# Kernel tuning notes

Hardware: AMD Instinct MI355X
Metric: run time of the kernel (lower is better)

The kernel has to match this reference:

```python
import jax, jax.numpy as jnp
import numpy as np

N_NODES = 50000
N_EDGES = 1_600_000


def gcn_conv(x, W, b, src, dst, ew, n_nodes):
    """PyG GCNConv: out = D^{-1/2}(A+I)D^{-1/2} (x W) + b, deg from edge_weight,
    self-loop weight = 1. Self-loop term handled analytically (norm = dinv[i]^2)."""
    xW = x @ W                                            # [N, F_out]
    deg = jax.ops.segment_sum(ew, dst, num_segments=n_nodes) + 1.0  # +1 self-loop
    dinv = jnp.where(deg > 0, jax.lax.rsqrt(deg), 0.0)    # [N]
    norm = dinv[src] * ew * dinv[dst]                     # [E]
    agg = jax.ops.segment_sum(norm[:, None] * xW[src], dst, num_segments=n_nodes)
    return agg + (dinv * dinv)[:, None] * xW + b


def setup_inputs() -> dict:
    key = jax.random.key(0)
    ks = jax.random.split(key, 9)
    s = lambda fi, fo: 1.0 / np.sqrt(fi)
    return {
        "x": jax.random.normal(ks[0], (N_NODES, 128), dtype=jnp.float32),
        "edge_index": jax.random.randint(ks[1], (2, N_EDGES), 0, N_NODES, dtype=jnp.int64)
        if jax.config.jax_enable_x64 else jax.random.randint(ks[1], (2, N_EDGES), 0, N_NODES, dtype=jnp.int32),
        "edge_weight": jax.random.uniform(ks[2], (N_EDGES,), dtype=jnp.float32),
        "W1": jax.random.normal(ks[3], (128, 64), dtype=jnp.float32) * s(128, 64),
        "b1": jnp.zeros((64,), dtype=jnp.float32),
        "W2": jax.random.normal(ks[4], (64, 64), dtype=jnp.float32) * s(64, 64),
        "b2": jnp.zeros((64,), dtype=jnp.float32),
        "W3": jax.random.normal(ks[5], (64, 40), dtype=jnp.float32) * s(64, 40),
        "b3": jnp.zeros((40,), dtype=jnp.float32),
    }


def reference(x, edge_index, edge_weight, W1, b1, W2, b2, W3, b3):
    src, dst = edge_index[0], edge_index[1]
    n = x.shape[0]
    h = jax.nn.relu(gcn_conv(x, W1, b1, src, dst, edge_weight, n))
    h = jax.nn.relu(gcn_conv(h, W2, b2, src, dst, edge_weight, n))
    return gcn_conv(h, W3, b3, src, dst, edge_weight, n)
```

## Files before the change

### kernel.cpp

```cpp
#include <hip/hip_runtime.h>


#define TILE 4096
#define BCAP_MAX 9216

typedef int s16i __attribute__((ext_vector_type(16)));

static __device__ __forceinline__ float4 f4zero() { return make_float4(0.f, 0.f, 0.f, 0.f); }

static __device__ __forceinline__ unsigned short f2bf_rne(float x) {
    unsigned u = __float_as_uint(x);
    u += 0x7FFFu + ((u >> 16) & 1u);
    return (unsigned short)(u >> 16);
}
static __device__ __forceinline__ float bf2f(unsigned short b) {
    return __uint_as_float((unsigned)b << 16);
}

__global__ __launch_bounds__(1024) void bin_count_kernel(
        const int* __restrict__ dst, int* __restrict__ cnt, int E, int ntiles) {
    __shared__ int h[256];
    const int tid = threadIdx.x;
    const int t = blockIdx.x;
    if (tid < 256) h[tid] = 0;
    __syncthreads();
    const int e0 = t * TILE;
    #pragma unroll
    for (int j = 0; j < 4; ++j) {
        int e = e0 + j * 1024 + tid;
        if (e < E) atomicAdd(&h[dst[e] >> 8], 1);
    }
    __syncthreads();
    if (tid < 256) cnt[tid * ntiles + t] = h[tid];
}

__global__ __launch_bounds__(512) void bin_scan_kernel(
        int* __restrict__ cnt, int* __restrict__ bintotal, int ntiles) {
    __shared__ int buf[512];
    const int b = blockIdx.x;
    const int tid = threadIdx.x;
    int v = (tid < ntiles) ? cnt[b * ntiles + tid] : 0;
    buf[tid] = v;
    __syncthreads();
    for (int off = 1; off < 512; off <<= 1) {
        int x = buf[tid];
        int a = (tid >= off) ? buf[tid - off] : 0;
        __syncthreads();
        buf[tid] = x + a;
        __syncthreads();
    }
    if (tid < ntiles) cnt[b * ntiles + tid] = buf[tid] - v;
    if (tid == 0) bintotal[b] = buf[511];
}

__global__ __launch_bounds__(1024) void bin_scatter_kernel(
        const int* __restrict__ src, const int* __restrict__ dst,
        const float* __restrict__ ew, const int* __restrict__ cntbase,
        int2* __restrict__ binned, int E, int bcap, int ntiles) {
    __shared__ int cnt[256];
    __shared__ int scan[256];
    __shared__ int gbase[256];
    __shared__ int2 sorted[TILE];
    __shared__ unsigned char binof[TILE];
    const int tid = threadIdx.x;
    const int t = blockIdx.x;
    const int e0 = t * TILE;

    if (tid < 256) cnt[tid] = 0;
    __syncthreads();

    int mypk[4]; float myew[4]; int mybin[4]; int myrank[4]; bool myok[4];
    #pragma unroll
    for (int j = 0; j < 4; ++j) {
        int e = e0 + j * 1024 + tid;
        myok[j] = (e < E);
        if (myok[j]) {
            int d = dst[e];
            int s = src[e];
            myew[j]   = ew[e];
            mybin[j]  = d >> 8;
            mypk[j]   = (s << 8) | (d & 255);
            myrank[j] = atomicAdd(&cnt[mybin[j]], 1);
        }
    }
    __syncthreads();
    if (tid < 256) scan[tid] = cnt[tid];
    __syncthreads();
    for (int off = 1; off < 256; off <<= 1) {
        int v = 0;
        if (tid < 256) { v = scan[tid]; if (tid >= off) v += scan[tid - off]; }
        __syncthreads();
        if (tid < 256) scan[tid] = v;
        __syncthreads();
    }
    if (tid < 256) gbase[tid] = cntbase[tid * ntiles + t];
    __syncthreads();
    #pragma unroll
    for (int j = 0; j < 4; ++j) {
        if (myok[j]) {
            int b = mybin[j];
            int slot = (scan[b] - cnt[b]) + myrank[j];
            sorted[slot] = make_int2(mypk[j], __float_as_int(myew[j]));
            binof[slot]  = (unsigned char)b;
        }
    }
    __syncthreads();
    const int total = scan[255];
    for (int i = tid; i < total; i += 1024) {
        int b = binof[i];
        int pos = gbase[b] + (i - (scan[b] - cnt[b]));
        if (pos < bcap)
            binned[(size_t)b * bcap + pos] = sorted[i];
    }
}

__global__ __launch_bounds__(1024) void bin_group_kernel(
        int2* __restrict__ binned, const int* __restrict__ bintotal,
        int* __restrict__ row_start, int* __restrict__ row_cnt,
        float* __restrict__ dinv, int N, int bcap) {
    __shared__ int   cntl[256];
    __shared__ float degl[256];
    __shared__ int   scan[256];
    __shared__ int   run[256];
    __shared__ int2  sorted[BCAP_MAX];
    const int b = blockIdx.x;
    const int tid = threadIdx.x;
    int n = bintotal[b];
    if (n > bcap) n = bcap;
    if (tid < 256) { cntl[tid] = 0; degl[tid] = 0.f; }
    __syncthreads();

    int2* seg = binned + (size_t)b * bcap;
    for (int i = tid; i < n; i += 1024) {
        int2 v = seg[i];
        int dl = v.x & 255;
        atomicAdd(&cntl[dl], 1);
        atomicAdd(&degl[dl], __int_as_float(v.y));
    }
    __syncthreads();
    if (tid < 256) scan[tid] = cntl[tid];
    __syncthreads();
    for (int off = 1; off < 256; off <<= 1) {
        int v = 0;
        if (tid < 256) { v = scan[tid]; if (tid >= off) v += scan[tid - off]; }
        __syncthreads();
        if (tid < 256) scan[tid] = v;
        __syncthreads();
    }
    if (tid < 256) {
        int ex = scan[tid] - cntl[tid];
        int d = (b << 8) + tid;
        if (d < N) {
            row_start[d] = b * bcap + ex;
            row_cnt[d]   = cntl[tid];
            dinv[d]      = rsqrtf(degl[tid] + 1.0f);
        }
        run[tid] = ex;
    }
    __syncthreads();
    for (int i = tid; i < n; i += 1024) {
        int2 v = seg[i];
        int dl = v.x & 255;
        int r = atomicAdd(&run[dl], 1);
        sorted[r] = make_int2((v.x >> 8) << 7, v.y);
    }
    __syncthreads();
    for (int i = tid; i < n; i += 1024)
        seg[i] = sorted[i];
}

template <int K, int M>
__global__ __launch_bounds__(256) void gemm_kernel(const float* __restrict__ X,
        const float* __restrict__ W, const float* __restrict__ dinv,
        unsigned short* __restrict__ Y, int N) {
    constexpr int KP = K + 4;
    __shared__ float xs[64 * KP];
    __shared__ float ws[K * M];
    const int tid = threadIdx.x;
    const int row0 = blockIdx.x * 64;

    for (int i = tid * 4; i < K * M; i += 1024)
        *(float4*)&ws[i] = *(const float4*)&W[i];

    const int nrows = min(64, N - row0);
    for (int i = tid * 4; i < 64 * K; i += 1024) {
        int r = i / K, k = i % K;
        float4 v = f4zero();
        if (r < nrows) v = *(const float4*)&X[(size_t)(row0 + r) * K + k];
        *(float4*)&xs[r * KP + k] = v;
    }
    __syncthreads();

    const int ct = tid & 15, rt = tid >> 4;
    const int c = ct * 4;
    const bool cok = (c < M);
    float acc[4][4] = {};
    for (int k = 0; k < K; ++k) {
        float a0 = xs[(rt +  0) * KP + k];
        float a1 = xs[(rt + 16) * KP + k];
        float a2 = xs[(rt + 32) * KP + k];
        float a3 = xs[(rt + 48) * KP + k];
        float4 bv = cok ? *(const float4*)&ws[k * M + c] : f4zero();
        acc[0][0] += a0 * bv.x; acc[0][1] += a0 * bv.y; acc[0][2] += a0 * bv.z; acc[0][3] += a0 * bv.w;
        acc[1][0] += a1 * bv.x; acc[1][1] += a1 * bv.y; acc[1][2] += a1 * bv.z; acc[1][3] += a1 * bv.w;
        acc[2][0] += a2 * bv.x; acc[2][1] += a2 * bv.y; acc[2][2] += a2 * bv.z; acc[2][3] += a2 * bv.w;
        acc[3][0] += a3 * bv.x; acc[3][1] += a3 * bv.y; acc[3][2] += a3 * bv.z; acc[3][3] += a3 * bv.w;
    }
    if (cok) {
        #pragma unroll
        for (int i = 0; i < 4; ++i) {
            int r = row0 + rt + 16 * i;
            if (r < N) {
                float dd = dinv[r];
                ushort4 o;
                o.x = f2bf_rne(acc[i][0] * dd); o.y = f2bf_rne(acc[i][1] * dd);
                o.z = f2bf_rne(acc[i][2] * dd); o.w = f2bf_rne(acc[i][3] * dd);
                *(ushort4*)&Y[(size_t)r * 64 + c] = o;
            }
        }
    }
}

template <int FOUT, bool RELU>
__global__ __launch_bounds__(256) void agg_kernel(
        const unsigned short* __restrict__ xw,
        const int2* __restrict__ csr, const int* __restrict__ row_start,
        const int* __restrict__ row_cnt, const float* __restrict__ dinv,
        const float* __restrict__ bias, float* __restrict__ out, int N) {
    int wid = (int)((blockIdx.x * blockDim.x + threadIdx.x) >> 6);
    int lane = threadIdx.x & 63;
    if (wid >= N) return;

    const unsigned rs  = (unsigned)__builtin_amdgcn_readfirstlane(row_start[wid]);
    const int      cnt = __builtin_amdgcn_readfirstlane(row_cnt[wid]);
    unsigned long long addr = (unsigned long long)csr + (unsigned long long)rs * 8ull;
    const char* xwb = (const char*)xw;

    float acc0 = 0.f, acc1 = 0.f;
    int j = 0;
    for (; j + 16 <= cnt; j += 16) {
        s16i edA, edB;
        asm volatile("s_load_dwordx16 %0, %2, 0x0\n\t"
                     "s_load_dwordx16 %1, %2, 0x40\n\t"
                     "s_waitcnt lgkmcnt(0)"
                     : "=&s"(edA), "=&s"(edB) : "s"(addr));
        #pragma unroll
        for (int p = 0; p < 8; ++p) {
            const unsigned short* pp = (const unsigned short*)(xwb + (unsigned)edA[2 * p]);
            float xv = bf2f(pp[lane]);
            float w  = __int_as_float(edA[2 * p + 1]);
            if (p & 1) acc1 = fmaf(w, xv, acc1); else acc0 = fmaf(w, xv, acc0);
        }
        #pragma unroll
        for (int p = 0; p < 8; ++p) {
            const unsigned short* pp = (const unsigned short*)(xwb + (unsigned)edB[2 * p]);
            float xv = bf2f(pp[lane]);
            float w  = __int_as_float(edB[2 * p + 1]);
            if (p & 1) acc1 = fmaf(w, xv, acc1); else acc0 = fmaf(w, xv, acc0);
        }
        addr += 128ull;
    }
    if (j < cnt) {
        const int r = cnt - j;
        s16i edA, edB;
        asm volatile("s_load_dwordx16 %0, %2, 0x0\n\t"
                     "s_load_dwordx16 %1, %2, 0x40\n\t"
                     "s_waitcnt lgkmcnt(0)"
                     : "=&s"(edA), "=&s"(edB) : "s"(addr));
        #pragma unroll
        for (int p = 0; p < 8; ++p) {
            if (p < r) {
                const unsigned short* pp = (const unsigned short*)(xwb + (unsigned)edA[2 * p]);
                float xv = bf2f(pp[lane]);
                float w  = __int_as_float(edA[2 * p + 1]);
                if (p & 1) acc1 = fmaf(w, xv, acc1); else acc0 = fmaf(w, xv, acc0);
            }
        }
        #pragma unroll
        for (int p = 0; p < 8; ++p) {
            if (p + 8 < r) {
                const unsigned short* pp = (const unsigned short*)(xwb + (unsigned)edB[2 * p]);
                float xv = bf2f(pp[lane]);
                float w  = __int_as_float(edB[2 * p + 1]);
                if (p & 1) acc1 = fmaf(w, xv, acc1); else acc0 = fmaf(w, xv, acc0);
            }
        }
    }

    if (lane < FOUT) {
        float dd = dinv[wid];
        float selfv = bf2f(xw[(size_t)wid * 64 + lane]);
        float v = dd * (acc0 + acc1 + selfv) + bias[lane];
        if (RELU) v = fmaxf(v, 0.f);
        out[(size_t)wid * FOUT + lane] = v;
    }
}

static inline size_t ws_align(size_t x) { return (x + 255) & ~(size_t)255; }

extern "C" void kernel_launch(void* const* d_in, const int* in_sizes, int n_in,
                              void* d_out, int out_size, void* d_ws, size_t ws_size,
                              hipStream_t stream) {
    const float* x  = (const float*)d_in[0];
    const int*   ei = (const int*)d_in[1];
    const float* ew = (const float*)d_in[2];
    const float* W1 = (const float*)d_in[3];
    const float* b1 = (const float*)d_in[4];
    const float* W2 = (const float*)d_in[5];
    const float* b2 = (const float*)d_in[6];
    const float* W3 = (const float*)d_in[7];
    const float* b3 = (const float*)d_in[8];
    float* out = (float*)d_out;

    const int N = in_sizes[0] / 128;
    const int E = in_sizes[1] / 2;
    const int* src = ei;
    const int* dst = ei + E;
    const int nbins = (N + 255) >> 8;
    const int ntiles = (E + TILE - 1) / TILE;

    char* p = (char*)d_ws;
    size_t off = 0;
    auto alloc = [&](size_t bytes) -> char* {
        char* q = p + off;
        off = ws_align(off + bytes);
        return q;
    };
    int*   row_start = (int*)  alloc((size_t)N * 4);
    int*   row_cnt   = (int*)  alloc((size_t)N * 4);
    float* dinv      = (float*)alloc((size_t)N * 4);
    int*   cntbase   = (int*)  alloc((size_t)256 * ntiles * 4);
    int*   bintotal  = (int*)  alloc((size_t)256 * 4);
    unsigned short* xwbuf = (unsigned short*)alloc((size_t)N * 64 * 2);
    float* hbuf      = (float*)alloc((size_t)N * 64 * 4);
    size_t remain = (ws_size > off + 512) ? (ws_size - off - 512) : 0;
    int bcap = (int)(remain / ((size_t)nbins * 8));
    if (bcap > BCAP_MAX) bcap = BCAP_MAX;
    int2* binned = (int2*)alloc((size_t)nbins * (size_t)bcap * 8);

    const int gb = (N + 63) / 64;
    const int ab = (N + 3) / 4;

    bin_count_kernel<<<ntiles, 1024, 0, stream>>>(dst, cntbase, E, ntiles);
    bin_scan_kernel<<<256, 512, 0, stream>>>(cntbase, bintotal, ntiles);
    bin_scatter_kernel<<<ntiles, 1024, 0, stream>>>(src, dst, ew, cntbase, binned, E, bcap, ntiles);
    bin_group_kernel<<<nbins, 1024, 0, stream>>>(binned, bintotal, row_start, row_cnt, dinv, N, bcap);

    gemm_kernel<128, 64><<<gb, 256, 0, stream>>>(x, W1, dinv, xwbuf, N);
    agg_kernel<64, true ><<<ab, 256, 0, stream>>>(xwbuf, binned, row_start, row_cnt, dinv, b1, hbuf, N);
    gemm_kernel<64, 64><<<gb, 256, 0, stream>>>(hbuf, W2, dinv, xwbuf, N);
    agg_kernel<64, true ><<<ab, 256, 0, stream>>>(xwbuf, binned, row_start, row_cnt, dinv, b2, hbuf, N);
    gemm_kernel<64, 40><<<gb, 256, 0, stream>>>(hbuf, W3, dinv, xwbuf, N);
    agg_kernel<40, false><<<ab, 256, 0, stream>>>(xwbuf, binned, row_start, row_cnt, dinv, b3, out, N);
}
```

Measured before the change: 293.4 us.

## Split wavefront into 8 edge groups with 16-byte row loads in aggregation

The aggregation kernel now lets each group of 8 lanes handle a different edge. Each lane loads 16 bytes (8 bf16 features) of a neighbour row, so a wavefront processes 8 edges per load instruction instead of one edge per 2-byte-per-lane load. Per-group partial sums are combined with xor-shuffle reductions, and the epilogue writes 8 outputs per lane with vector stores. This cuts the number of memory instructions and adds per-edge select logic plus a shuffle reduction. FOUT=40 relies on 40 being divisible by 8.

```diff
diff --git a/kernel.cpp b/kernel.cpp
--- a/kernel.cpp
+++ b/kernel.cpp
@@ -13,8 +13,19 @@
     u += 0x7FFFu + ((u >> 16) & 1u);
     return (unsigned short)(u >> 16);
 }
-static __device__ __forceinline__ float bf2f(unsigned short b) {
-    return __uint_as_float((unsigned)b << 16);
+static __device__ __forceinline__ float bflo(unsigned u) { return __uint_as_float(u << 16); }
+static __device__ __forceinline__ float bfhi(unsigned u) { return __uint_as_float(u & 0xffff0000u); }
+
+static __device__ __forceinline__ unsigned sel8(bool b3, bool b4, bool b5,
+        unsigned e0, unsigned e1, unsigned e2, unsigned e3,
+        unsigned e4, unsigned e5, unsigned e6, unsigned e7) {
+    unsigned a  = b3 ? e1 : e0;
+    unsigned b  = b3 ? e3 : e2;
+    unsigned c  = b3 ? e5 : e4;
+    unsigned d  = b3 ? e7 : e6;
+    unsigned ab = b4 ? b : a;
+    unsigned cd = b4 ? d : c;
+    return b5 ? cd : ab;
 }
 
 __global__ __launch_bounds__(1024) void bin_count_kernel(
@@ -236,7 +247,14 @@
     unsigned long long addr = (unsigned long long)csr + (unsigned long long)rs * 8ull;
     const char* xwb = (const char*)xw;
 
-    float acc0 = 0.f, acc1 = 0.f;
+    const int g = lane >> 3;
+    const unsigned li16 = (unsigned)(lane & 7) * 16u;
+    const bool b3 = (lane & 8)  != 0;
+    const bool b4 = (lane & 16) != 0;
+    const bool b5 = (lane & 32) != 0;
+
+    float acc[8] = {0.f, 0.f, 0.f, 0.f, 0.f, 0.f, 0.f, 0.f};
+
     int j = 0;
     for (; j + 16 <= cnt; j += 16) {
         s16i edA, edB;
@@ -244,55 +262,118 @@
                      "s_load_dwordx16 %1, %2, 0x40\n\t"
                      "s_waitcnt lgkmcnt(0)"
                      : "=&s"(edA), "=&s"(edB) : "s"(addr));
-        #pragma unroll
-        for (int p = 0; p < 8; ++p) {
-            const unsigned short* pp = (const unsigned short*)(xwb + (unsigned)edA[2 * p]);
-            float xv = bf2f(pp[lane]);
-            float w  = __int_as_float(edA[2 * p + 1]);
-            if (p & 1) acc1 = fmaf(w, xv, acc1); else acc0 = fmaf(w, xv, acc0);
-        }
-        #pragma unroll
-        for (int p = 0; p < 8; ++p) {
-            const unsigned short* pp = (const unsigned short*)(xwb + (unsigned)edB[2 * p]);
-            float xv = bf2f(pp[lane]);
-            float w  = __int_as_float(edB[2 * p + 1]);
-            if (p & 1) acc1 = fmaf(w, xv, acc1); else acc0 = fmaf(w, xv, acc0);
+        {
+            unsigned off = sel8(b3, b4, b5,
+                (unsigned)edA[0], (unsigned)edA[2], (unsigned)edA[4], (unsigned)edA[6],
+                (unsigned)edA[8], (unsigned)edA[10], (unsigned)edA[12], (unsigned)edA[14]);
+            float wf = __uint_as_float(sel8(b3, b4, b5,
+                (unsigned)edA[1], (unsigned)edA[3], (unsigned)edA[5], (unsigned)edA[7],
+                (unsigned)edA[9], (unsigned)edA[11], (unsigned)edA[13], (unsigned)edA[15]));
+            uint4 row = *(const uint4*)(xwb + (off + li16));
+            acc[0] = fmaf(wf, bflo(row.x), acc[0]);
+            acc[1] = fmaf(wf, bfhi(row.x), acc[1]);
+            acc[2] = fmaf(wf, bflo(row.y), acc[2]);
+            acc[3] = fmaf(wf, bfhi(row.y), acc[3]);
+            acc[4] = fmaf(wf, bflo(row.z), acc[4]);
+            acc[5] = fmaf(wf, bfhi(row.z), acc[5]);
+            acc[6] = fmaf(wf, bflo(row.w), acc[6]);
+            acc[7] = fmaf(wf, bfhi(row.w), acc[7]);
+        }
+        {
+            unsigned off = sel8(b3, b4, b5,
+                (unsigned)edB[0], (unsigned)edB[2], (unsigned)edB[4], (unsigned)edB[6],
+                (unsigned)edB[8], (unsigned)edB[10], (unsigned)edB[12], (unsigned)edB[14]);
+            float wf = __uint_as_float(sel8(b3, b4, b5,
+                (unsigned)edB[1], (unsigned)edB[3], (unsigned)edB[5], (unsigned)edB[7],
+                (unsigned)edB[9], (unsigned)edB[11], (unsigned)edB[13], (unsigned)edB[15]));
+            uint4 row = *(const uint4*)(xwb + (off + li16));
+            acc[0] = fmaf(wf, bflo(row.x), acc[0]);
+            acc[1] = fmaf(wf, bfhi(row.x), acc[1]);
+            acc[2] = fmaf(wf, bflo(row.y), acc[2]);
+            acc[3] = fmaf(wf, bfhi(row.y), acc[3]);
+            acc[4] = fmaf(wf, bflo(row.z), acc[4]);
+            acc[5] = fmaf(wf, bfhi(row.z), acc[5]);
+            acc[6] = fmaf(wf, bflo(row.w), acc[6]);
+            acc[7] = fmaf(wf, bfhi(row.w), acc[7]);
         }
         addr += 128ull;
     }
     if (j < cnt) {
-        const int r = cnt - j;
+        const int rem = cnt - j;
         s16i edA, edB;
         asm volatile("s_load_dwordx16 %0, %2, 0x0\n\t"
                      "s_load_dwordx16 %1, %2, 0x40\n\t"
                      "s_waitcnt lgkmcnt(0)"
                      : "=&s"(edA), "=&s"(edB) : "s"(addr));
+        {
+            unsigned off = sel8(b3, b4, b5,
+                (unsigned)edA[0], (unsigned)edA[2], (unsigned)edA[4], (unsigned)edA[6],
+                (unsigned)edA[8], (unsigned)edA[10], (unsigned)edA[12], (unsigned)edA[14]);
+            float wf = __uint_as_float(sel8(b3, b4, b5,
+                (unsigned)edA[1], (unsigned)edA[3], (unsigned)edA[5], (unsigned)edA[7],
+                (unsigned)edA[9], (unsigned)edA[11], (unsigned)edA[13], (unsigned)edA[15]));
+            bool valid = (g < rem);
+            off = valid ? off : 0u;
+            wf  = valid ? wf : 0.f;
+            uint4 row = *(const uint4*)(xwb + (off + li16));
+            acc[0] = fmaf(wf, bflo(row.x), acc[0]);
+            acc[1] = fmaf(wf, bfhi(row.x), acc[1]);
+            acc[2] = fmaf(wf, bflo(row.y), acc[2]);
+            acc[3] = fmaf(wf, bfhi(row.y), acc[3]);
+            acc[4] = fmaf(wf, bflo(row.z), acc[4]);
+            acc[5] = fmaf(wf, bfhi(row.z), acc[5]);
+            acc[6] = fmaf(wf, bflo(row.w), acc[6]);
+            acc[7] = fmaf(wf, bfhi(row.w), acc[7]);
+        }
+        if (rem > 8) {
+            unsigned off = sel8(b3, b4, b5,
+                (unsigned)edB[0], (unsigned)edB[2], (unsigned)edB[4], (unsigned)edB[6],
+                (unsigned)edB[8], (unsigned)edB[10], (unsigned)edB[12], (unsigned)edB[14]);
+            float wf = __uint_as_float(sel8(b3, b4, b5,
+                (unsigned)edB[1], (unsigned)edB[3], (unsigned)edB[5], (unsigned)edB[7],
+                (unsigned)edB[9], (unsigned)edB[11], (unsigned)edB[13], (unsigned)edB[15]));
+            bool valid = (g + 8 < rem);
+            off = valid ? off : 0u;
+            wf  = valid ? wf : 0.f;
+            uint4 row = *(const uint4*)(xwb + (off + li16));
+            acc[0] = fmaf(wf, bflo(row.x), acc[0]);
+            acc[1] = fmaf(wf, bfhi(row.x), acc[1]);
+            acc[2] = fmaf(wf, bflo(row.y), acc[2]);
+            acc[3] = fmaf(wf, bfhi(row.y), acc[3]);
+            acc[4] = fmaf(wf, bflo(row.z), acc[4]);
+            acc[5] = fmaf(wf, bfhi(row.z), acc[5]);
+            acc[6] = fmaf(wf, bflo(row.w), acc[6]);
+            acc[7] = fmaf(wf, bfhi(row.w), acc[7]);
+        }
+    }
+
+    #pragma unroll
+    for (int o = 8; o <= 32; o <<= 1) {
         #pragma unroll
-        for (int p = 0; p < 8; ++p) {
-            if (p < r) {
-                const unsigned short* pp = (const unsigned short*)(xwb + (unsigned)edA[2 * p]);
-                float xv = bf2f(pp[lane]);
-                float w  = __int_as_float(edA[2 * p + 1]);
-                if (p & 1) acc1 = fmaf(w, xv, acc1); else acc0 = fmaf(w, xv, acc0);
-            }
-        }
-        #pragma unroll
-        for (int p = 0; p < 8; ++p) {
-            if (p + 8 < r) {
-                const unsigned short* pp = (const unsigned short*)(xwb + (unsigned)edB[2 * p]);
-                float xv = bf2f(pp[lane]);
-                float w  = __int_as_float(edB[2 * p + 1]);
-                if (p & 1) acc1 = fmaf(w, xv, acc1); else acc0 = fmaf(w, xv, acc0);
-            }
-        }
-    }
-
-    if (lane < FOUT) {
+        for (int t = 0; t < 8; ++t)
+            acc[t] += __shfl_xor(acc[t], o);
+    }
+
+    if (lane < FOUT / 8) {
+        const int f0 = lane * 8;
+        uint4 sr = *(const uint4*)(xwb + ((unsigned)wid * 128u + li16));
         float dd = dinv[wid];
-        float selfv = bf2f(xw[(size_t)wid * 64 + lane]);
-        float v = dd * (acc0 + acc1 + selfv) + bias[lane];
-        if (RELU) v = fmaxf(v, 0.f);
-        out[(size_t)wid * FOUT + lane] = v;
+        float4 bv0 = *(const float4*)&bias[f0];
+        float4 bv1 = *(const float4*)&bias[f0 + 4];
+        float r0 = dd * (acc[0] + bflo(sr.x)) + bv0.x;
+        float r1 = dd * (acc[1] + bfhi(sr.x)) + bv0.y;
+        float r2 = dd * (acc[2] + bflo(sr.y)) + bv0.z;
+        float r3 = dd * (acc[3] + bfhi(sr.y)) + bv0.w;
+        float r4 = dd * (acc[4] + bflo(sr.z)) + bv1.x;
+        float r5 = dd * (acc[5] + bfhi(sr.z)) + bv1.y;
+        float r6 = dd * (acc[6] + bflo(sr.w)) + bv1.z;
+        float r7 = dd * (acc[7] + bfhi(sr.w)) + bv1.w;
+        if (RELU) {
+            r0 = fmaxf(r0, 0.f); r1 = fmaxf(r1, 0.f); r2 = fmaxf(r2, 0.f); r3 = fmaxf(r3, 0.f);
+            r4 = fmaxf(r4, 0.f); r5 = fmaxf(r5, 0.f); r6 = fmaxf(r6, 0.f); r7 = fmaxf(r7, 0.f);
+        }
+        *(float4*)&out[(size_t)wid * FOUT + f0]     = make_float4(r0, r1, r2, r3);
+        *(float4*)&out[(size_t)wid * FOUT + f0 + 4] = make_float4(r4, r5, r6, r7);
     }
 }
 
```

Result: faster. 266.9 us (-9.0%).
